# Kernel optimization log

Hardware: AMD Instinct MI355X
Metric: run time of the kernel (lower is better)

The kernel has to match this reference:

```python
import jax, jax.numpy as jnp
from jax import lax
import numpy as np

D_MODEL = 512
D_STATE = 16
DI = 1024        # expand * d_model
DT_RANK = 32     # ceil(d_model/16)
K = 4            # mamba d_conv
NC = 8           # n_clusters
B = 2
L = 1024
EPS_LN = 1e-5


def _ln(x, g, b):
    m = jnp.mean(x, axis=-1, keepdims=True)
    v = jnp.mean((x - m) ** 2, axis=-1, keepdims=True)
    return (x - m) / jnp.sqrt(v + EPS_LN) * g + b


def _l2norm(x):
    n = jnp.linalg.norm(x, axis=-1, keepdims=True)
    return x / jnp.maximum(n, 1e-12)


def _ssm_scan(dA, dBu, C):
    # dA, dBu: (B, L, DI, N); C: (B, L, N) -> y: (B, L, DI)
    def step(h, inp):
        dA_t, dBu_t, c_t = inp
        h = dA_t * h + dBu_t                      # (B, DI, N)
        y = jnp.einsum('bdn,bn->bd', h, c_t)      # (B, DI)
        return h, y
    h0 = jnp.zeros((dA.shape[0], dA.shape[2], dA.shape[3]), dA.dtype)
    _, ys = lax.scan(step, h0, (jnp.swapaxes(dA, 0, 1), jnp.swapaxes(dBu, 0, 1), jnp.swapaxes(C, 0, 1)))
    return jnp.swapaxes(ys, 0, 1)


def _mamba(x, in_w, conv_w, conv_b, xproj_w, dt_w, dt_b, A_log, Dp, out_w):
    # x: (B, L, d_model)
    xz = x @ in_w.T                               # (B, L, 2*DI)
    xp, z = jnp.split(xz, 2, axis=-1)
    # depthwise causal conv1d
    xc = lax.conv_general_dilated(jnp.swapaxes(xp, 1, 2), conv_w, (1,), [(K - 1, 0)], feature_group_count=DI)
    xc = jax.nn.silu(xc + conv_b[None, :, None])
    xc = jnp.swapaxes(xc, 1, 2)                   # (B, L, DI)
    x_dbl = xc @ xproj_w.T                        # (B, L, DT_RANK + 2*N)
    dt, Bm, Cm = jnp.split(x_dbl, [DT_RANK, DT_RANK + D_STATE], axis=-1)
    delta = jax.nn.softplus(dt @ dt_w.T + dt_b)   # (B, L, DI)
    A = -jnp.exp(A_log)                           # (DI, N)
    dA = jnp.exp(delta[..., None] * A)            # (B, L, DI, N)
    dBu = (delta * xc)[..., None] * Bm[:, :, None, :]
    y = _ssm_scan(dA, dBu, Cm) + xc * Dp
    y = y * jax.nn.silu(z)
    return y @ out_w.T


def _forward(x, norm1_g, norm1_b,
             fm_in_w, fm_conv_w, fm_conv_b, fm_xproj_w, fm_dt_w, fm_dt_b, fm_A_log, fm_D, fm_out_w,
             bm_in_w, bm_conv_w, bm_conv_b, bm_xproj_w, bm_dt_w, bm_dt_b, bm_A_log, bm_D, bm_out_w,
             fusion_w, fusion_b, cc_centers, cc_proj_w, cc_proj_b, cc_norm_g, cc_norm_b, cc_alpha,
             gate_w, gate_b, ffn_norm_g, ffn_norm_b, ffn_w1, ffn_b1, ffn_w2, ffn_b2):
    xn = _ln(x, norm1_g, norm1_b)
    # bidirectional mamba path
    f_out = _mamba(xn, fm_in_w, fm_conv_w, fm_conv_b, fm_xproj_w, fm_dt_w, fm_dt_b, fm_A_log, fm_D, fm_out_w)
    b_out = jnp.flip(_mamba(jnp.flip(xn, axis=1), bm_in_w, bm_conv_w, bm_conv_b, bm_xproj_w, bm_dt_w, bm_dt_b, bm_A_log, bm_D, bm_out_w), axis=1)
    mamba_out = jnp.concatenate([f_out, b_out], axis=-1) @ fusion_w.T + fusion_b
    # context clustering path (dropout = identity at eval)
    proj = xn @ cc_proj_w.T + cc_proj_b
    sim = jnp.einsum('bld,cd->blc', _l2norm(proj), _l2norm(cc_centers))
    w = jax.nn.softmax(sim, axis=-1)
    ctx = jnp.einsum('blc,cd->bld', w, cc_centers)
    cc_out = _ln(xn + cc_alpha * ctx, cc_norm_g, cc_norm_b)
    # gated fusion
    g = jax.nn.softmax(xn @ gate_w.T + gate_b, axis=-1)  # (B, L, 2)
    fused = g[..., 0:1] * mamba_out + g[..., 1:2] * cc_out
    x = x + fused
    h = _ln(x, ffn_norm_g, ffn_norm_b)
    h = jax.nn.gelu(h @ ffn_w1.T + ffn_b1, approximate=False) @ ffn_w2.T + ffn_b2
    return x + h


def setup_inputs() -> dict:
    key = jax.random.key(0)
    ks = iter(jax.random.split(key, 64))
    nrm = lambda shape, s=0.02: jax.random.normal(next(ks), shape, jnp.float32) * s

    def mamba_params():
        A_log = jnp.tile(jnp.log(jnp.arange(1, D_STATE + 1, dtype=jnp.float32))[None, :], (DI, 1))
        return dict(in_w=nrm((2 * DI, D_MODEL)), conv_w=nrm((DI, 1, K), 0.1), conv_b=jnp.zeros((DI,)),
                    xproj_w=nrm((DT_RANK + 2 * D_STATE, DI)), dt_w=nrm((DI, DT_RANK), 0.1),
                    dt_b=nrm((DI,), 0.1), A_log=A_log, D=jnp.ones((DI,)), out_w=nrm((D_MODEL, DI)))

    fm = mamba_params()
    bm = mamba_params()
    d = {
        'x': jax.random.normal(next(ks), (B, L, D_MODEL), jnp.float32),
        'norm1_g': jnp.ones((D_MODEL,)), 'norm1_b': jnp.zeros((D_MODEL,)),
        'fusion_w': nrm((D_MODEL, 2 * D_MODEL)), 'fusion_b': jnp.zeros((D_MODEL,)),
        'cc_centers': jax.random.normal(next(ks), (NC, D_MODEL), jnp.float32),
        'cc_proj_w': nrm((D_MODEL, D_MODEL)), 'cc_proj_b': jnp.zeros((D_MODEL,)),
        'cc_norm_g': jnp.ones((D_MODEL,)), 'cc_norm_b': jnp.zeros((D_MODEL,)),
        'cc_alpha': jnp.array([0.05], jnp.float32),
        'gate_w': nrm((2, D_MODEL)), 'gate_b': jnp.zeros((2,)),
        'ffn_norm_g': jnp.ones((D_MODEL,)), 'ffn_norm_b': jnp.zeros((D_MODEL,)),
        'ffn_w1': nrm((4 * D_MODEL, D_MODEL)), 'ffn_b1': jnp.zeros((4 * D_MODEL,)),
        'ffn_w2': nrm((D_MODEL, 4 * D_MODEL)), 'ffn_b2': jnp.zeros((D_MODEL,)),
    }
    for pfx, p in (('fm', fm), ('bm', bm)):
        for k, v in p.items():
            d[pfx + '_' + k] = v
    return d


def reference(x, norm1_g, norm1_b,
              fm_in_w, fm_conv_w, fm_conv_b, fm_xproj_w, fm_dt_w, fm_dt_b, fm_A_log, fm_D, fm_out_w,
              bm_in_w, bm_conv_w, bm_conv_b, bm_xproj_w, bm_dt_w, bm_dt_b, bm_A_log, bm_D, bm_out_w,
              fusion_w, fusion_b, cc_centers, cc_proj_w, cc_proj_b, cc_norm_g, cc_norm_b, cc_alpha,
              gate_w, gate_b, ffn_norm_g, ffn_norm_b, ffn_w1, ffn_b1, ffn_w2, ffn_b2):
    return _forward(x, norm1_g, norm1_b,
                    fm_in_w, fm_conv_w, fm_conv_b, fm_xproj_w, fm_dt_w, fm_dt_b, fm_A_log, fm_D, fm_out_w,
                    bm_in_w, bm_conv_w, bm_conv_b, bm_xproj_w, bm_dt_w, bm_dt_b, bm_A_log, bm_D, bm_out_w,
                    fusion_w, fusion_b, cc_centers, cc_proj_w, cc_proj_b, cc_norm_g, cc_norm_b, cc_alpha,
                    gate_w, gate_b, ffn_norm_g, ffn_norm_b, ffn_w1, ffn_b1, ffn_w2, ffn_b2)
```

## Files before the change

### kernel.cpp

```cpp
#include <hip/hip_runtime.h>
#include <hip/hip_bf16.h>
#include <hip/hip_fp16.h>
#include <math.h>

using bf16 = __hip_bfloat16;

typedef __attribute__((ext_vector_type(8))) short v8s;
typedef __attribute__((ext_vector_type(4))) short v4s;
typedef __attribute__((ext_vector_type(4))) float v4f;

constexpr int kB   = 2;
constexpr int kL   = 1024;
constexpr int kD   = 512;
constexpr int kDI  = 1024;
constexpr int kNS  = 16;
constexpr int kDTR = 32;
constexpr int kKC  = 4;
constexpr int kNC  = 8;
constexpr int kM   = kB * kL;
constexpr int kCH  = 32;
constexpr int kCL  = kL / kCH;
constexpr float kEPS = 1e-5f;

static __device__ __forceinline__ float toF(bf16 x) { return __bfloat162float(x); }
static __device__ __forceinline__ float b2f(short u) {
    unsigned int x = ((unsigned int)(unsigned short)u) << 16;
    return __uint_as_float(x);
}

static __device__ __forceinline__ float ldin(const void* p, int i, int f32) {
    if (f32) return ((const float*)p)[i];
    return toF(((const bf16*)p)[i]);
}

static __device__ __forceinline__ int flipL(int r) { return r ^ (kL - 1); }

static __device__ __forceinline__ float blockReduceSum(float v, float* s) {
    __syncthreads();
#pragma unroll
    for (int o = 32; o > 0; o >>= 1) v += __shfl_down(v, o, 64);
    int lane = threadIdx.x & 63, wid = threadIdx.x >> 6;
    if (lane == 0) s[wid] = v;
    __syncthreads();
    if (threadIdx.x == 0) {
        float t = 0.f;
        for (int i = 0; i < 4; ++i) t += s[i];
        s[4] = t;
    }
    __syncthreads();
    return s[4];
}

static __device__ __forceinline__ int detect_local(const unsigned short* x, float* sred) {
    float c = 0.f;
    for (int i = threadIdx.x; i < 512; i += 256) {
        unsigned short h = x[2 * i];
        int e = (h >> 7) & 0xFF;
        if (e >= 100 && e <= 140) c += 1.f;
    }
    float tot = blockReduceSum(c, sred);
    return (tot >= 256.f) ? 0 : 1;
}

struct WSrcs { const void* p[12]; };

__global__ __launch_bounds__(256) void setup_kernel(WSrcs s, bf16* __restrict__ dst,
                                                    const void* __restrict__ alog_f,
                                                    const void* __restrict__ alog_b,
                                                    const void* __restrict__ centers,
                                                    float* __restrict__ anT,
                                                    float* __restrict__ cn,
                                                    int* __restrict__ flag,
                                                    const unsigned short* __restrict__ x0) {
    __shared__ float sred[8];
    int f32 = detect_local(x0, sred);
    int t = blockIdx.y;
    if (t < 12) {
        const int sz[12]  = {1048576, 1048576, 65536, 65536, 32768, 32768,
                             524288, 524288, 524288, 262144, 1048576, 1048576};
        const int off[12] = {0, 1048576, 2097152, 2162688, 2228224, 2260992,
                             2293760, 2818048, 3342336, 3866624, 4128768, 5177344};
        int n = sz[t];
        const void* src = s.p[t];
        bf16* d = dst + off[t];
        for (int i = blockIdx.x * 256 + threadIdx.x; i < n; i += 512 * 256)
            d[i] = __float2bfloat16(ldin(src, i, f32));
    } else {
        int bx = blockIdx.x;
        if (bx < 128) {
            int tid = bx * 256 + threadIdx.x;
            int d = tid & (kDI - 1);
            int n = (tid >> 10) & (kNS - 1);
            int dir = tid >> 14;
            anT[tid] = -__expf(ldin(dir ? alog_b : alog_f, d * kNS + n, f32));
        } else if (bx < 136) {
            int c = bx - 128;
            float ssum = 0.f;
            for (int i = threadIdx.x; i < kD; i += 256) {
                float v = ldin(centers, c * kD + i, f32);
                ssum += v * v;
            }
            float tot = blockReduceSum(ssum, sred);
            if (threadIdx.x == 0) cn[c] = sqrtf(tot);
        } else if (bx == 136) {
            if (threadIdx.x == 0) *flag = f32;
        }
    }
}

__global__ __launch_bounds__(256) void ln_in_kernel(const void* __restrict__ X,
                                                    const void* __restrict__ g,
                                                    const void* __restrict__ b,
                                                    bf16* __restrict__ Y,
                                                    const int* __restrict__ flg) {
    __shared__ float sred[8];
    int f32 = *flg;
    int row = blockIdx.x;
    int i = threadIdx.x;
    size_t base = (size_t)row * kD;
    float x0 = ldin(X, base + i, f32), x1 = ldin(X, base + i + 256, f32);
    float mean = blockReduceSum(x0 + x1, sred) * (1.f / kD);
    float vs = blockReduceSum(x0 * x0 + x1 * x1, sred) * (1.f / kD) - mean * mean;
    float rstd = rsqrtf(vs + kEPS);
    Y[base + i]       = __float2bfloat16((x0 - mean) * rstd * ldin(g, i, f32)       + ldin(b, i, f32));
    Y[base + i + 256] = __float2bfloat16((x1 - mean) * rstd * ldin(g, i + 256, f32) + ldin(b, i + 256, f32));
}

template <int BM, int BN, int WRN, int WCN>
__global__ __launch_bounds__(256) void mfma_gemm(const bf16* __restrict__ A, int lda, int aZOff,
                                                 const bf16* __restrict__ W, int K, int wZOff,
                                                 const void* __restrict__ bias, int act,
                                                 const float* __restrict__ resid,
                                                 bf16* __restrict__ outB,
                                                 void* __restrict__ outRaw,
                                                 int ldo, int oZOff,
                                                 int flipN0, int zflip,
                                                 const int* __restrict__ flg,
                                                 bf16* __restrict__ outSplitZ,
                                                 const bf16* __restrict__ wCcp,
                                                 const void* __restrict__ ccpBias,
                                                 bf16* __restrict__ outCcp,
                                                 int nSplit2) {
    __shared__ bf16 As[BM * 64];
    __shared__ bf16 Bs[BN * 64];
    constexpr int FR = BM / WRN / 16;
    constexpr int FC = BN / WCN / 16;
    constexpr int AV = BM / 32;
    constexpr int BV = BN / 32;

    int f32 = *flg;
    int tid = threadIdx.x;
    int z = blockIdx.z;
    const bf16* Ab = A + (size_t)z * aZOff;
    int m0 = blockIdx.y * BM, n0 = blockIdx.x * BN;
    const bf16* Wb = W + (size_t)z * wZOff;
    int nrow0 = n0;
    bool isCcp = (wCcp != nullptr) && (n0 >= nSplit2);
    if (isCcp) { Wb = wCcp; nrow0 = n0 - nSplit2; }
    int lane = tid & 63, w = tid >> 6;
    int wr = w % WRN, wc = w / WRN;
    int rbase = wr * (BM / WRN), cbase = wc * (BN / WCN);
    int quad = lane >> 4, lrow = lane & 15;
    int wbase = tid & ~63;

    v4f acc[FR][FC];
#pragma unroll
    for (int i = 0; i < FR; ++i)
#pragma unroll
        for (int j = 0; j < FC; ++j)
#pragma unroll
            for (int r = 0; r < 4; ++r) acc[i][j][r] = 0.f;

    for (int kt = 0; kt < K; kt += 64) {
#pragma unroll
        for (int i = 0; i < AV; ++i) {
            int v = i * 256 + tid;
            int row = v >> 3;
            int c8 = ((v & 7) * 8) ^ ((row & 7) * 8);
            const bf16* gp = Ab + (size_t)(m0 + row) * lda + kt + c8;
            __builtin_amdgcn_global_load_lds(
                (const __attribute__((address_space(1))) void*)gp,
                (__attribute__((address_space(3))) void*)&As[(i * 256 + wbase) * 8],
                16, 0, 0);
        }
#pragma unroll
        for (int i = 0; i < BV; ++i) {
            int v = i * 256 + tid;
            int row = v >> 3;
            int c8 = ((v & 7) * 8) ^ ((row & 7) * 8);
            const bf16* gp = Wb + (size_t)(nrow0 + row) * K + kt + c8;
            __builtin_amdgcn_global_load_lds(
                (const __attribute__((address_space(1))) void*)gp,
                (__attribute__((address_space(3))) void*)&Bs[(i * 256 + wbase) * 8],
                16, 0, 0);
        }
        __syncthreads();
#pragma unroll
        for (int k0 = 0; k0 < 64; k0 += 32) {
            v8s a[FR], b[FC];
#pragma unroll
            for (int fr = 0; fr < FR; ++fr) {
                int r = rbase + fr * 16 + lrow;
                a[fr] = *reinterpret_cast<const v8s*>(
                    &As[r * 64 + ((k0 + quad * 8) ^ ((r & 7) * 8))]);
            }
#pragma unroll
            for (int fc = 0; fc < FC; ++fc) {
                int r = cbase + fc * 16 + lrow;
                b[fc] = *reinterpret_cast<const v8s*>(
                    &Bs[r * 64 + ((k0 + quad * 8) ^ ((r & 7) * 8))]);
            }
#pragma unroll
            for (int fr = 0; fr < FR; ++fr)
#pragma unroll
                for (int fc = 0; fc < FC; ++fc)
                    acc[fr][fc] = __builtin_amdgcn_mfma_f32_16x16x32_bf16(a[fr], b[fc], acc[fr][fc], 0, 0, 0);
        }
        __syncthreads();
    }

    bf16* outBz = outB ? outB + (size_t)z * oZOff : nullptr;
#pragma unroll
    for (int fr = 0; fr < FR; ++fr) {
#pragma unroll
        for (int fc = 0; fc < FC; ++fc) {
            int ncol = n0 + cbase + fc * 16 + lrow;
            float bi = bias ? ldin(bias, ncol, f32) : 0.f;
            bool doflip = (ncol >= flipN0) || (zflip && z == 1);
#pragma unroll
            for (int r = 0; r < 4; ++r) {
                int m = m0 + rbase + fr * 16 + quad * 4 + r;
                float vv = acc[fr][fc][r] + bi;
                if (act == 2) vv = 0.5f * vv * (1.f + erff(vv * 0.70710678118654752440f));
                if (resid) vv += resid[(size_t)m * ldo + ncol];
                if (outCcp && ncol >= nSplit2) {
                    float v2 = vv + ldin(ccpBias, ncol - nSplit2, f32);
                    outCcp[(size_t)m * kD + (ncol - nSplit2)] = __float2bfloat16(v2);
                } else if (outSplitZ) {
                    int dir = (ncol >> 11) & 1;
                    int isz = (ncol >> 10) & 1;
                    int c2 = dir * 1024 + (ncol & 1023);
                    int mo_ = dir ? flipL(m) : m;
                    bf16* dst = isz ? outSplitZ : outB;
                    dst[(size_t)mo_ * 2048 + c2] = __float2bfloat16(vv);
                } else {
                    int mo_ = doflip ? flipL(m) : m;
                    size_t oi = (size_t)mo_ * ldo + ncol;
                    if (outBz) outBz[oi] = __float2bfloat16(vv);
                    else if (f32) ((float*)outRaw)[oi] = vv;
                    else ((bf16*)outRaw)[oi] = __float2bfloat16(vv);
                }
            }
        }
    }
}

__global__ __launch_bounds__(256) void conv_kernel(const bf16* __restrict__ xp,
                                                   const void* __restrict__ cw_f,
                                                   const void* __restrict__ cb_f,
                                                   const void* __restrict__ cw_b,
                                                   const void* __restrict__ cb_b,
                                                   bf16* __restrict__ xc,
                                                   const int* __restrict__ flg) {
    int f32 = *flg;
    int tid = blockIdx.x * 256 + threadIdx.x;
    int d = tid & (kDI - 1);
    int r = (tid >> 10) & (kM - 1);
    int dir = tid >> 21;
    int l = r & (kL - 1);
    int b = r >> 10;
    const void* cw = dir ? cw_b : cw_f;
    const void* cb = dir ? cb_b : cb_f;
    float acc = ldin(cb, d, f32);
#pragma unroll
    for (int k = 0; k < kKC; ++k) {
        int ll = l - (kKC - 1) + k;
        if (ll >= 0)
            acc += ldin(cw, d * kKC + k, f32) *
                   toF(xp[(size_t)(b * kL + ll) * (2 * kDI) + dir * kDI + d]);
    }
    float s = acc / (1.f + __expf(-acc));
    xc[(size_t)r * (2 * kDI) + dir * kDI + d] = __float2bfloat16(s);
}

__global__ __launch_bounds__(256) void delta_kernel(const bf16* __restrict__ xdbl,
                                                    const bf16* __restrict__ wdt,
                                                    const void* __restrict__ dtb_f,
                                                    const void* __restrict__ dtb_b,
                                                    __half* __restrict__ deltaH,
                                                    const int* __restrict__ flg) {
    __shared__ float arow[kDTR];
    int f32 = *flg;
    int m = blockIdx.y;
    int dir = blockIdx.z;
    int d = blockIdx.x * 256 + threadIdx.x;
    if (threadIdx.x < kDTR)
        arow[threadIdx.x] = toF(xdbl[(size_t)m * 128 + dir * 64 + threadIdx.x]);
    __syncthreads();
    float acc = ldin(dir ? dtb_b : dtb_f, d, f32);
    const v8s* wv = reinterpret_cast<const v8s*>(wdt + ((size_t)dir * kDI + d) * kDTR);
#pragma unroll
    for (int t = 0; t < 4; ++t) {
        v8s w8 = wv[t];
#pragma unroll
        for (int k = 0; k < 8; ++k) acc += arow[t * 8 + k] * b2f(w8[k]);
    }
    acc = (acc > 20.f) ? acc : log1pf(__expf(acc));
    deltaH[((size_t)dir * kM + m) * kDI + d] = __float2half(acc);
}

__global__ __launch_bounds__(256) void scan_phase1(const bf16* __restrict__ xc,
                                                   const bf16* __restrict__ xdbl,
                                                   __half* __restrict__ deltaS,
                                                   const float* __restrict__ anT,
                                                   float* __restrict__ PA,
                                                   __half* __restrict__ HLh,
                                                   bf16* __restrict__ ymul,
                                                   const int* __restrict__ flg) {
    int tid = blockIdx.x * 256 + threadIdx.x;
    int n4  = tid & 3;
    int d   = (tid >> 2) & (kDI - 1);
    int c   = (tid >> 12) & (kCH - 1);
    int b   = (tid >> 17) & 1;
    int dir = tid >> 18;
    float an[4], h[4], pa[4];
#pragma unroll
    for (int j = 0; j < 4; ++j) {
        an[j] = anT[((size_t)dir * kNS + n4 * 4 + j) * kDI + d];
        h[j] = 0.f;
        pa[j] = 1.f;
    }
    __half* dptr = deltaS + ((size_t)dir * kM + (size_t)b * kL) * kDI + d;
    float s = 0.f;
    int l0 = c * kCL;
    for (int l = l0; l < l0 + kCL; ++l) {
        size_t rb = (size_t)b * kL + l;
        float dl = __half2float(dptr[(size_t)l * kDI]);
        s += dl;
        float xcv = toF(xc[rb * (2 * kDI) + dir * kDI + d]);
        float du = dl * xcv;
        v4s Bv = *reinterpret_cast<const v4s*>(xdbl + rb * 128 + dir * 64 + kDTR + n4 * 4);
        v4s Cv = *reinterpret_cast<const v4s*>(xdbl + rb * 128 + dir * 64 + kDTR + kNS + n4 * 4);
        float yp = 0.f;
#pragma unroll
        for (int j = 0; j < 4; ++j) {
            float a = __expf(dl * an[j]);
            pa[j] *= a;
            h[j] = a * h[j] + du * b2f(Bv[j]);
            yp += h[j] * b2f(Cv[j]);
        }
        yp += __shfl_xor(yp, 1);
        yp += __shfl_xor(yp, 2);
        if (n4 == 0) {
            ymul[rb * (2 * kDI) + dir * kDI + d] = __float2bfloat16(yp);
            dptr[(size_t)l * kDI] = __float2half(s);
        }
    }
    int g = dir * kB + b;
    size_t o = (((size_t)g * kCH + c) * kNS + n4 * 4) * kDI + d;
#pragma unroll
    for (int j = 0; j < 4; ++j) {
        PA[o + (size_t)j * kDI] = pa[j];
        HLh[o + (size_t)j * kDI] = __float2half(h[j]);
    }
}

__global__ __launch_bounds__(256) void scan_phase2(float* __restrict__ PA,
                                                   const __half* __restrict__ HLh) {
    int tid = blockIdx.x * 256 + threadIdx.x;
    int d = tid & (kDI - 1);
    int n = (tid >> 10) & (kNS - 1);
    int g = tid >> 14;
    float h = 0.f;
    for (int c = 0; c < kCH; ++c) {
        size_t idx = (((size_t)g * kCH + c) * kNS + n) * kDI + d;
        float pav = PA[idx];
        float hlv = __half2float(HLh[idx]);
        PA[idx] = h;
        h = pav * h + hlv;
    }
}

__global__ __launch_bounds__(256) void scan_fix(const bf16* __restrict__ xc,
                                                const bf16* __restrict__ xdbl,
                                                const bf16* __restrict__ zb,
                                                const __half* __restrict__ sbuf,
                                                const float* __restrict__ anT,
                                                const void* __restrict__ dp_f,
                                                const void* __restrict__ dp_b,
                                                const float* __restrict__ HIN,
                                                bf16* __restrict__ ymul,
                                                const int* __restrict__ flg) {
    int f32 = *flg;
    int tid = blockIdx.x * 256 + threadIdx.x;
    int d   = tid & (kDI - 1);
    int l   = (tid >> 10) & (kL - 1);
    int b   = (tid >> 20) & 1;
    int dir = tid >> 21;
    int c   = l / kCL;
    size_t rb = (size_t)b * kL + l;
    float s = __half2float(sbuf[((size_t)dir * kM + rb) * kDI + d]);
    int g = dir * kB + b;
    const float* hin = HIN + (((size_t)g * kCH + c) * kNS) * kDI + d;
    const float* anp = anT + (size_t)dir * kNS * kDI + d;
    const bf16* Cp = xdbl + rb * 128 + dir * 64 + kDTR + kNS;
    float ycorr = 0.f;
#pragma unroll
    for (int n = 0; n < kNS; ++n) {
        float an = anp[(size_t)n * kDI];
        ycorr += toF(Cp[n]) * __expf(an * s) * hin[(size_t)n * kDI];
    }
    size_t yi = rb * (2 * kDI) + dir * kDI + d;
    float xcv = toF(xc[yi]);
    float Dv = ldin(dir ? dp_b : dp_f, d, f32);
    float y = toF(ymul[yi]) + ycorr + xcv * Dv;
    float zv = toF(zb[yi]);
    float sz = zv / (1.f + __expf(-zv));
    ymul[yi] = __float2bfloat16(y * sz);
}

__global__ __launch_bounds__(256) void post_kernel(const bf16* __restrict__ proj,
                                                   const void* __restrict__ centers,
                                                   const float* __restrict__ cn,
                                                   const bf16* __restrict__ xn,
                                                   const void* __restrict__ alpha_p,
                                                   const void* __restrict__ ccg,
                                                   const void* __restrict__ ccb,
                                                   const void* __restrict__ X,
                                                   const bf16* __restrict__ mo,
                                                   const void* __restrict__ gw,
                                                   const void* __restrict__ gb,
                                                   const void* __restrict__ fg,
                                                   const void* __restrict__ fbb,
                                                   float* __restrict__ xmid,
                                                   bf16* __restrict__ hln,
                                                   const int* __restrict__ flg) {
    __shared__ float sred[8];
    __shared__ float sims[kNC];
    int f32 = *flg;
    int row = blockIdx.x;
    int i = threadIdx.x;
    size_t base = (size_t)row * kD;
    float p0 = toF(proj[base + i]), p1 = toF(proj[base + i + 256]);
    float sumsq = blockReduceSum(p0 * p0 + p1 * p1, sred);
    float pn = fmaxf(sqrtf(sumsq), 1e-12f);
    for (int c = 0; c < kNC; ++c) {
        float part = p0 * ldin(centers, c * kD + i, f32) + p1 * ldin(centers, c * kD + i + 256, f32);
        float dot = blockReduceSum(part, sred);
        if (threadIdx.x == 0) sims[c] = dot / (pn * fmaxf(cn[c], 1e-12f));
    }
    __syncthreads();
    float mx = -1e30f;
#pragma unroll
    for (int c = 0; c < kNC; ++c) mx = fmaxf(mx, sims[c]);
    float wv[kNC], se = 0.f;
#pragma unroll
    for (int c = 0; c < kNC; ++c) { wv[c] = __expf(sims[c] - mx); se += wv[c]; }
    float inv = 1.f / se;
    float ctx0 = 0.f, ctx1 = 0.f;
#pragma unroll
    for (int c = 0; c < kNC; ++c) {
        float wc = wv[c] * inv;
        ctx0 += wc * ldin(centers, c * kD + i, f32);
        ctx1 += wc * ldin(centers, c * kD + i + 256, f32);
    }
    float alpha = ldin(alpha_p, 0, f32);
    float x0 = toF(xn[base + i]), x1 = toF(xn[base + i + 256]);
    float t0 = x0 + alpha * ctx0;
    float t1 = x1 + alpha * ctx1;
    float mean = blockReduceSum(t0 + t1, sred) * (1.f / kD);
    float vs = blockReduceSum(t0 * t0 + t1 * t1, sred) * (1.f / kD) - mean * mean;
    float rstd = rsqrtf(vs + kEPS);
    float cc0 = (t0 - mean) * rstd * ldin(ccg, i, f32)       + ldin(ccb, i, f32);
    float cc1 = (t1 - mean) * rstd * ldin(ccg, i + 256, f32) + ldin(ccb, i + 256, f32);
    float d0 = blockReduceSum(x0 * ldin(gw, i, f32) + x1 * ldin(gw, i + 256, f32), sred);
    float d1 = blockReduceSum(x0 * ldin(gw, kD + i, f32) + x1 * ldin(gw, kD + i + 256, f32), sred);
    d0 += ldin(gb, 0, f32);
    d1 += ldin(gb, 1, f32);
    float gmx = fmaxf(d0, d1);
    float e0 = __expf(d0 - gmx), e1 = __expf(d1 - gmx);
    float gs = e0 + e1;
    float g0 = e0 / gs, g1 = e1 / gs;
    float xm0 = ldin(X, base + i, f32)       + g0 * toF(mo[base + i])       + g1 * cc0;
    float xm1 = ldin(X, base + i + 256, f32) + g0 * toF(mo[base + i + 256]) + g1 * cc1;
    xmid[base + i] = xm0;
    xmid[base + i + 256] = xm1;
    float mean2 = blockReduceSum(xm0 + xm1, sred) * (1.f / kD);
    float vs2 = blockReduceSum(xm0 * xm0 + xm1 * xm1, sred) * (1.f / kD) - mean2 * mean2;
    float rstd2 = rsqrtf(vs2 + kEPS);
    hln[base + i]       = __float2bfloat16((xm0 - mean2) * rstd2 * ldin(fg, i, f32)       + ldin(fbb, i, f32));
    hln[base + i + 256] = __float2bfloat16((xm1 - mean2) * rstd2 * ldin(fg, i + 256, f32) + ldin(fbb, i + 256, f32));
}

extern "C" void kernel_launch(void* const* d_in, const int* in_sizes, int n_in,
                              void* d_out, int out_size, void* d_ws, size_t ws_size,
                              hipStream_t stream) {
    bool sig = (n_in > 3 && in_sizes[3] == 2 * kDI * kD);
    int I_fusion_w = sig ? 21 : 3,  I_fusion_b = sig ? 22 : 4;
    int I_centers  = sig ? 23 : 5,  I_ccp_w    = sig ? 24 : 6,  I_ccp_b = sig ? 25 : 7;
    int I_ccn_g    = sig ? 26 : 8,  I_ccn_b    = sig ? 27 : 9,  I_alpha = sig ? 28 : 10;
    int I_gate_w   = sig ? 29 : 11, I_gate_b   = sig ? 30 : 12;
    int I_ffn_g    = sig ? 31 : 13, I_ffn_b    = sig ? 32 : 14;
    int I_ffn_w1   = sig ? 33 : 15, I_ffn_b1   = sig ? 34 : 16;
    int I_ffn_w2   = sig ? 35 : 17, I_ffn_b2   = sig ? 36 : 18;
    int I_fm       = sig ? 3  : 19, I_bm       = sig ? 12 : 28;

    const void* X        = d_in[0];
    const void* n1g      = d_in[1];
    const void* n1b      = d_in[2];
    const void* fusion_b = d_in[I_fusion_b];
    const void* centers  = d_in[I_centers];
    const void* ccp_b    = d_in[I_ccp_b];
    const void* ccn_g    = d_in[I_ccn_g];
    const void* ccn_b    = d_in[I_ccn_b];
    const void* cc_alpha = d_in[I_alpha];
    const void* gate_w   = d_in[I_gate_w];
    const void* gate_b   = d_in[I_gate_b];
    const void* ffn_g    = d_in[I_ffn_g];
    const void* ffn_b    = d_in[I_ffn_b];
    const void* ffn_b1   = d_in[I_ffn_b1];
    const void* ffn_b2   = d_in[I_ffn_b2];

    float* ws = (float*)d_ws;
    int* flg  = (int*)d_ws;
    float* cn = ws + 8;
    float*  anT  = ws + 32;
    float*  PA   = anT + 32768;
    __half* HLh  = (__half*)(PA + 2097152);
    bf16*  xn   = (bf16*)((float*)HLh + 1048576);
    bf16*  xp   = (bf16*)((float*)xn + 524288);
    bf16*  zb   = (bf16*)((float*)xp + 2097152);
    bf16*  xc   = (bf16*)((float*)zb + 2097152);
    bf16*  xdbl = (bf16*)((float*)xc + 2097152);
    bf16*  ymul = (bf16*)((float*)xdbl + 131072);
    bf16*  wbuf = (bf16*)((float*)ymul + 2097152);
    bf16*  projb = (bf16*)((float*)wbuf + 3112960);
    __half* deltaH = (__half*)xp;
    bf16*  fb    = (bf16*)HLh;
    bf16*  mo    = (bf16*)PA;
    float* xmid  = PA + 524288;
    bf16*  hln   = xc;
    bf16*  ffnh  = zb;

    bf16* w_in     = wbuf + 0;
    bf16* w_xp     = wbuf + 2097152;
    bf16* w_dt     = wbuf + 2228224;
    bf16* w_out    = wbuf + 2293760;
    bf16* w_fusion = wbuf + 3342336;
    bf16* w_ccp    = wbuf + 3866624;
    bf16* w_ffn1   = wbuf + 4128768;
    bf16* w_ffn2   = wbuf + 5177344;

    dim3 blk(256);
    constexpr int NOFLIP = 1 << 30;

    WSrcs srcs;
    srcs.p[0] = d_in[I_fm + 0]; srcs.p[1] = d_in[I_bm + 0];
    srcs.p[2] = d_in[I_fm + 3]; srcs.p[3] = d_in[I_bm + 3];
    srcs.p[4] = d_in[I_fm + 4]; srcs.p[5] = d_in[I_bm + 4];
    srcs.p[6] = d_in[I_fm + 8]; srcs.p[7] = d_in[I_bm + 8];
    srcs.p[8] = d_in[I_fusion_w]; srcs.p[9] = d_in[I_ccp_w];
    srcs.p[10] = d_in[I_ffn_w1]; srcs.p[11] = d_in[I_ffn_w2];

    setup_kernel<<<dim3(512, 13), blk, 0, stream>>>(
        srcs, wbuf, d_in[I_fm + 6], d_in[I_bm + 6], centers, anT, cn, flg,
        (const unsigned short*)X);

    ln_in_kernel<<<kM, blk, 0, stream>>>(X, n1g, n1b, xn, flg);

    mfma_gemm<128, 64, 2, 2><<<dim3(72, 16, 1), blk, 0, stream>>>(
        xn, kD, 0, w_in, kD, 0, nullptr, 0, nullptr, xp, nullptr, 2048, 0, NOFLIP, 0, flg, zb,
        w_ccp, ccp_b, projb, 4096);

    conv_kernel<<<2 * kM * kDI / 256, blk, 0, stream>>>(
        xp, d_in[I_fm + 1], d_in[I_fm + 2], d_in[I_bm + 1], d_in[I_bm + 2], xc, flg);

    mfma_gemm<32, 64, 1, 4><<<dim3(1, 64, 2), blk, 0, stream>>>(
        xc, 2 * kDI, kDI, w_xp, kDI, 65536, nullptr, 0, nullptr, xdbl, nullptr, 128, 64,
        NOFLIP, 0, flg, nullptr, nullptr, nullptr, nullptr, NOFLIP);

    delta_kernel<<<dim3(kDI / 256, kM, 2), blk, 0, stream>>>(
        xdbl, w_dt, d_in[I_fm + 5], d_in[I_bm + 5], deltaH, flg);

    scan_phase1<<<2048, blk, 0, stream>>>(xc, xdbl, deltaH, anT, PA, HLh, ymul, flg);
    scan_phase2<<<256, blk, 0, stream>>>(PA, HLh);
    scan_fix<<<16384, blk, 0, stream>>>(xc, xdbl, zb, deltaH, anT,
                                        d_in[I_fm + 7], d_in[I_bm + 7], PA, ymul, flg);

    mfma_gemm<32, 64, 1, 4><<<dim3(8, 64, 2), blk, 0, stream>>>(
        ymul, 2 * kDI, kDI, w_out, kDI, 524288, nullptr, 0, nullptr, fb, nullptr, 2 * kD, kD,
        NOFLIP, 1, flg, nullptr, nullptr, nullptr, nullptr, NOFLIP);

    mfma_gemm<32, 64, 1, 4><<<dim3(8, 64, 1), blk, 0, stream>>>(
        fb, 2 * kD, 0, w_fusion, 2 * kD, 0, fusion_b, 0, nullptr, mo, nullptr, kD, 0,
        NOFLIP, 0, flg, nullptr, nullptr, nullptr, nullptr, NOFLIP);

    post_kernel<<<kM, blk, 0, stream>>>(projb, centers, cn, xn, cc_alpha, ccn_g, ccn_b,
                                        X, mo, gate_w, gate_b, ffn_g, ffn_b, xmid, hln, flg);

    mfma_gemm<64, 64, 2, 2><<<dim3(32, 32, 1), blk, 0, stream>>>(
        hln, kD, 0, w_ffn1, kD, 0, ffn_b1, 2, nullptr, ffnh, nullptr, 4 * kD, 0, NOFLIP, 0, flg,
        nullptr, nullptr, nullptr, nullptr, NOFLIP);
    mfma_gemm<32, 64, 1, 4><<<dim3(8, 64, 1), blk, 0, stream>>>(
        ffnh, 4 * kD, 0, w_ffn2, 4 * kD, 0, ffn_b2, 0, xmid, nullptr, d_out, kD, 0,
        NOFLIP, 0, flg, nullptr, nullptr, nullptr, nullptr, NOFLIP);
}
```

Measured before the change: 375.8 us.

## Fuse input layernorm into setup kernel and x_proj GEMM with delta projection

```diff
diff --git a/kernel.cpp b/kernel.cpp
--- a/kernel.cpp
+++ b/kernel.cpp
@@ -71,9 +71,12 @@
                                                     float* __restrict__ anT,
                                                     float* __restrict__ cn,
                                                     int* __restrict__ flag,
-                                                    const unsigned short* __restrict__ x0) {
+                                                    const void* __restrict__ X,
+                                                    const void* __restrict__ n1g,
+                                                    const void* __restrict__ n1b,
+                                                    bf16* __restrict__ xn) {
     __shared__ float sred[8];
-    int f32 = detect_local(x0, sred);
+    int f32 = detect_local((const unsigned short*)X, sred);
     int t = blockIdx.y;
     if (t < 12) {
         const int sz[12]  = {1048576, 1048576, 65536, 65536, 32768, 32768,
@@ -85,7 +88,7 @@
         bf16* d = dst + off[t];
         for (int i = blockIdx.x * 256 + threadIdx.x; i < n; i += 512 * 256)
             d[i] = __float2bfloat16(ldin(src, i, f32));
-    } else {
+    } else if (t == 12) {
         int bx = blockIdx.x;
         if (bx < 128) {
             int tid = bx * 256 + threadIdx.x;
@@ -105,25 +108,17 @@
         } else if (bx == 136) {
             if (threadIdx.x == 0) *flag = f32;
         }
-    }
-}
-
-__global__ __launch_bounds__(256) void ln_in_kernel(const void* __restrict__ X,
-                                                    const void* __restrict__ g,
-                                                    const void* __restrict__ b,
-                                                    bf16* __restrict__ Y,
-                                                    const int* __restrict__ flg) {
-    __shared__ float sred[8];
-    int f32 = *flg;
-    int row = blockIdx.x;
-    int i = threadIdx.x;
-    size_t base = (size_t)row * kD;
-    float x0 = ldin(X, base + i, f32), x1 = ldin(X, base + i + 256, f32);
-    float mean = blockReduceSum(x0 + x1, sred) * (1.f / kD);
-    float vs = blockReduceSum(x0 * x0 + x1 * x1, sred) * (1.f / kD) - mean * mean;
-    float rstd = rsqrtf(vs + kEPS);
-    Y[base + i]       = __float2bfloat16((x0 - mean) * rstd * ldin(g, i, f32)       + ldin(b, i, f32));
-    Y[base + i + 256] = __float2bfloat16((x1 - mean) * rstd * ldin(g, i + 256, f32) + ldin(b, i + 256, f32));
+    } else {
+        int row = (t - 13) * 512 + blockIdx.x;
+        int i = threadIdx.x;
+        size_t base = (size_t)row * kD;
+        float x0 = ldin(X, base + i, f32), x1 = ldin(X, base + i + 256, f32);
+        float mean = blockReduceSum(x0 + x1, sred) * (1.f / kD);
+        float vs = blockReduceSum(x0 * x0 + x1 * x1, sred) * (1.f / kD) - mean * mean;
+        float rstd = rsqrtf(vs + kEPS);
+        xn[base + i]       = __float2bfloat16((x0 - mean) * rstd * ldin(n1g, i, f32)       + ldin(n1b, i, f32));
+        xn[base + i + 256] = __float2bfloat16((x1 - mean) * rstd * ldin(n1g, i + 256, f32) + ldin(n1b, i + 256, f32));
+    }
 }
 
 template <int BM, int BN, int WRN, int WCN>
@@ -283,30 +278,59 @@
     xc[(size_t)r * (2 * kDI) + dir * kDI + d] = __float2bfloat16(s);
 }
 
-__global__ __launch_bounds__(256) void delta_kernel(const bf16* __restrict__ xdbl,
-                                                    const bf16* __restrict__ wdt,
-                                                    const void* __restrict__ dtb_f,
-                                                    const void* __restrict__ dtb_b,
-                                                    __half* __restrict__ deltaH,
-                                                    const int* __restrict__ flg) {
-    __shared__ float arow[kDTR];
+__global__ __launch_bounds__(256) void xproj_delta_kernel(
+    const bf16* __restrict__ xc,
+    const bf16* __restrict__ w_xp,
+    const bf16* __restrict__ w_dt,
+    const void* __restrict__ dtb_f,
+    const void* __restrict__ dtb_b,
+    bf16* __restrict__ xdbl,
+    __half* __restrict__ deltaH,
+    const int* __restrict__ flg) {
+    __shared__ bf16 xrow[2 * kDI];
+    __shared__ float xd[128];
     int f32 = *flg;
-    int m = blockIdx.y;
-    int dir = blockIdx.z;
-    int d = blockIdx.x * 256 + threadIdx.x;
-    if (threadIdx.x < kDTR)
-        arow[threadIdx.x] = toF(xdbl[(size_t)m * 128 + dir * 64 + threadIdx.x]);
+    int m = blockIdx.x;
+    int t = threadIdx.x;
+    {
+        v8s v = *reinterpret_cast<const v8s*>(xc + (size_t)m * (2 * kDI) + t * 8);
+        *reinterpret_cast<v8s*>(&xrow[t * 8]) = v;
+    }
     __syncthreads();
-    float acc = ldin(dir ? dtb_b : dtb_f, d, f32);
-    const v8s* wv = reinterpret_cast<const v8s*>(wdt + ((size_t)dir * kDI + d) * kDTR);
-#pragma unroll
-    for (int t = 0; t < 4; ++t) {
-        v8s w8 = wv[t];
-#pragma unroll
-        for (int k = 0; k < 8; ++k) acc += arow[t * 8 + k] * b2f(w8[k]);
-    }
-    acc = (acc > 20.f) ? acc : log1pf(__expf(acc));
-    deltaH[((size_t)dir * kM + m) * kDI + d] = __float2half(acc);
+    {
+        int o = t >> 1, half = t & 1;
+        int dir = o >> 6, n = o & 63;
+        const bf16* wrow = w_xp + ((size_t)dir * 64 + n) * kDI + half * 512;
+        const bf16* xsrc = &xrow[dir * kDI + half * 512];
+        float p = 0.f;
+#pragma unroll 8
+        for (int k = 0; k < 512; k += 8) {
+            v8s wv = *reinterpret_cast<const v8s*>(wrow + k);
+            v8s xv = *reinterpret_cast<const v8s*>(xsrc + k);
+#pragma unroll
+            for (int j = 0; j < 8; ++j) p += b2f(xv[j]) * b2f(wv[j]);
+        }
+        p += __shfl_xor(p, 1);
+        if (half == 0) {
+            xd[o] = p;
+            xdbl[(size_t)m * 128 + o] = __float2bfloat16(p);
+        }
+    }
+    __syncthreads();
+    for (int i = t; i < 2 * kDI; i += 256) {
+        int dir = i >> 10, d = i & (kDI - 1);
+        float acc = ldin(dir ? dtb_b : dtb_f, d, f32);
+        const bf16* wrow = w_dt + ((size_t)dir * kDI + d) * kDTR;
+        const float* xsrc = &xd[dir * 64];
+#pragma unroll
+        for (int kk = 0; kk < kDTR; kk += 8) {
+            v8s wv = *reinterpret_cast<const v8s*>(wrow + kk);
+#pragma unroll
+            for (int j = 0; j < 8; ++j) acc += xsrc[kk + j] * b2f(wv[j]);
+        }
+        acc = (acc > 20.f) ? acc : log1pf(__expf(acc));
+        deltaH[((size_t)dir * kM + m) * kDI + d] = __float2half(acc);
+    }
 }
 
 __global__ __launch_bounds__(256) void scan_phase1(const bf16* __restrict__ xc,
@@ -562,11 +586,9 @@
     srcs.p[8] = d_in[I_fusion_w]; srcs.p[9] = d_in[I_ccp_w];
     srcs.p[10] = d_in[I_ffn_w1]; srcs.p[11] = d_in[I_ffn_w2];
 
-    setup_kernel<<<dim3(512, 13), blk, 0, stream>>>(
+    setup_kernel<<<dim3(512, 17), blk, 0, stream>>>(
         srcs, wbuf, d_in[I_fm + 6], d_in[I_bm + 6], centers, anT, cn, flg,
-        (const unsigned short*)X);
-
-    ln_in_kernel<<<kM, blk, 0, stream>>>(X, n1g, n1b, xn, flg);
+        X, n1g, n1b, xn);
 
     mfma_gemm<128, 64, 2, 2><<<dim3(72, 16, 1), blk, 0, stream>>>(
         xn, kD, 0, w_in, kD, 0, nullptr, 0, nullptr, xp, nullptr, 2048, 0, NOFLIP, 0, flg, zb,
@@ -575,12 +597,8 @@
     conv_kernel<<<2 * kM * kDI / 256, blk, 0, stream>>>(
         xp, d_in[I_fm + 1], d_in[I_fm + 2], d_in[I_bm + 1], d_in[I_bm + 2], xc, flg);
 
-    mfma_gemm<32, 64, 1, 4><<<dim3(1, 64, 2), blk, 0, stream>>>(
-        xc, 2 * kDI, kDI, w_xp, kDI, 65536, nullptr, 0, nullptr, xdbl, nullptr, 128, 64,
-        NOFLIP, 0, flg, nullptr, nullptr, nullptr, nullptr, NOFLIP);
-
-    delta_kernel<<<dim3(kDI / 256, kM, 2), blk, 0, stream>>>(
-        xdbl, w_dt, d_in[I_fm + 5], d_in[I_bm + 5], deltaH, flg);
+    xproj_delta_kernel<<<kM, blk, 0, stream>>>(
+        xc, w_xp, w_dt, d_in[I_fm + 5], d_in[I_bm + 5], xdbl, deltaH, flg);
 
     scan_phase1<<<2048, blk, 0, stream>>>(xc, xdbl, deltaH, anT, PA, HLh, ymul, flg);
     scan_phase2<<<256, blk, 0, stream>>>(PA, HLh);
```

New measurement: 449.7 us. +19.7%, slower.
